# Kernel optimization log

Hardware: AMD Instinct MI355X
Metric: run time of the kernel (lower is better)

Reference implementation:

```python
import jax, jax.numpy as jnp
import numpy as np

ALPHA = 1.0
RANK = 4


def _conv2d_same(x, w):
    # x: [B,C,H,W], w: [O,C,kh,kw], stride 1, 'same' padding
    return jax.lax.conv_general_dilated(
        x, w, window_strides=(1, 1), padding='SAME',
        dimension_numbers=('NCHW', 'OIHW', 'NCHW'))


def setup_inputs() -> dict:
    key = jax.random.key(0)
    k1, k2, k3, k4, k5 = jax.random.split(key, 5)
    B, C, H, W = 32, 64, 64, 256
    O, E, r, k = 64, 4, RANK, 3
    x = jax.random.normal(k1, (B, C, H, W), dtype=jnp.float32)
    subject_id = jax.random.randint(k2, (B,), 0, E, dtype=jnp.int64)
    W_conv = jax.random.normal(k3, (O, C, k, k), dtype=jnp.float32) * (1.0 / np.sqrt(C * k * k))
    W_A = jax.random.normal(k4, (E, r, C, k, k), dtype=jnp.float32) * 0.02
    # torch init zeros W_B; use random here so the LoRA path is numerically exercised
    W_B = jax.random.normal(k5, (E, O, r), dtype=jnp.float32) * 0.02
    return {'x': x, 'subject_id': subject_id, 'W_conv': W_conv, 'W_A': W_A, 'W_B': W_B}


def reference(x, subject_id, W_conv, W_A, W_B):
    B, C, H, W = x.shape
    E, r = W_A.shape[0], W_A.shape[1]
    k = W_A.shape[-1]
    # Base conv
    out = _conv2d_same(x, W_conv)  # [B,O,H,W]
    # Run all adapter A-convs in one batched conv (E*r tiny output channels),
    # then per-sample select the adapter matching subject_id (same math as the
    # masked per-adapter dispatch in the original).
    a_all = _conv2d_same(x, W_A.reshape(E * r, C, k, k))  # [B,E*r,H,W]
    a_all = a_all.reshape(B, E, r, H, W)
    idx = subject_id[:, None, None, None, None]
    a_sel = jnp.take_along_axis(a_all, idx, axis=1)[:, 0]  # [B,r,H,W]
    wb_sel = W_B[subject_id]  # [B,O,r] (1x1 conv weight per sample)
    lora = (ALPHA / r) * jnp.einsum('bor,brhw->bohw', wb_sel, a_sel)
    return out + lora
```

## Files before the change

kernel.cpp:

```cpp
#include <hip/hip_runtime.h>
#include <hip/hip_bf16.h>

typedef __attribute__((ext_vector_type(8)))  short bf16x8;
typedef __attribute__((ext_vector_type(16))) float f32x16;

constexpr int Bn = 32, Cn = 64, Hn = 64, Wn = 256, On = 64, En = 4, Rn = 4;
constexpr float SCALE = 1.0f / Rn;

constexpr int ROW_B  = 258 * 128;

constexpr int WTILE  = 64;
constexpr int HSTRIP = 8;
constexpr int SLOT_B = 66 * 128;

constexpr size_t WFRAG_B = 294912;
constexpr size_t XP_B    = (size_t)Bn * Hn * ROW_B;
constexpr size_t ZROW_B  = ROW_B;

#define GLOAD_LDS16(SRC, DST) \
    __builtin_amdgcn_global_load_lds( \
        (const __attribute__((address_space(1))) void*)(SRC), \
        (__attribute__((address_space(3))) void*)(DST), 16, 0, 0)

__global__ __launch_bounds__(256) void merge_k(
    const float* __restrict__ Wc, const float* __restrict__ Wa,
    const float* __restrict__ Wb, __hip_bfloat16* __restrict__ Wfrag)
{
    int t = blockIdx.x * 256 + threadIdx.x;
    int j    = t & 7;
    int lane = (t >> 3) & 63;
    int g    = t >> 9;
    int s    = g % 36;
    int mh   = (g / 36) & 1;
    int e    = g / 72;
    int m = lane & 31, half = lane >> 5;
    int o = mh * 32 + m;
    int tap = s >> 2, cq = s & 3;
    int c = cq * 16 + half * 8 + j;
    float acc = Wc[(o * Cn + c) * 9 + tap];
#pragma unroll
    for (int r = 0; r < Rn; ++r)
        acc += SCALE * Wb[(e * On + o) * Rn + r] * Wa[((e * Rn + r) * Cn + c) * 9 + tap];
    Wfrag[t] = __float2bfloat16(acc);
}

__global__ __launch_bounds__(256) void pack2_k(
    const float* __restrict__ x, __hip_bfloat16* __restrict__ xp,
    __hip_bfloat16* __restrict__ zr)
{
    const int blk = blockIdx.x;
    if (blk < 4096) {
        int l  = ((blk & 1) << 8) | threadIdx.x;
        int bh = blk >> 1;
        int wLo = l & 3, cb = (l >> 2) & 7, wHi = l >> 5;
        int wq = wHi * 4 + wLo;
        int b = bh >> 6, h = bh & 63;
        const float* src = x + (((size_t)(b * Cn + cb * 8) * Hn + h) * Wn) + 4 * wq;
        float4 f[8];
#pragma unroll
        for (int i = 0; i < 8; ++i)
            f[i] = *reinterpret_cast<const float4*>(src + (size_t)i * Hn * Wn);
        char* row = (char*)xp + (size_t)bh * ROW_B;
#pragma unroll
        for (int j = 0; j < 4; ++j) {
            union { __hip_bfloat16 u[8]; bf16x8 v; } pk;
#pragma unroll
            for (int i = 0; i < 8; ++i) {
                float v = (j == 0) ? f[i].x : (j == 1) ? f[i].y : (j == 2) ? f[i].z : f[i].w;
                pk.u[i] = __float2bfloat16(v);
            }
            int s = 4 * wq + 1 + j;
            *reinterpret_cast<bf16x8*>(row + s * 128 + ((cb ^ (s & 7)) * 16)) = pk.v;
        }
    } else if (blk < 4096 + 128) {
        int z = (blk - 4096) * 256 + threadIdx.x;
        int cb = z & 7, t = (z >> 3) & 1, bh = z >> 4;
        char* row = (char*)xp + (size_t)bh * ROW_B;
        bf16x8 zz = {};
        *reinterpret_cast<bf16x8*>(row + (t ? 257 : 0) * 128 + cb * 16) = zz;
    } else {
        int t = (blk - 4096 - 128) * 256 + threadIdx.x;
        if (t < ROW_B / 16) {
            bf16x8 zz = {};
            reinterpret_cast<bf16x8*>(zr)[t] = zz;
        }
    }
}

__global__ __launch_bounds__(256, 2) void conv10_k(
    const __hip_bfloat16* __restrict__ xp, const __hip_bfloat16* __restrict__ zr,
    const int* __restrict__ sid, const __hip_bfloat16* __restrict__ Wfrag,
    float* __restrict__ out)
{
    __shared__ __align__(16) char xs[4 * SLOT_B];

    const int logical = ((blockIdx.x & 7) << 7) | (blockIdx.x >> 3);
    const int bx = logical & 3, by = (logical >> 2) & 7, b = logical >> 5;

    const int tid = threadIdx.x;
    const int w0  = bx * WTILE;
    const int h0  = by * HSTRIP;
    const int e   = sid[b];
    const size_t HW = (size_t)Hn * Wn;

    const int lane = tid & 63, wave = tid >> 6;
    const int mh = wave & 1, nh = wave >> 1;
    const int n = lane & 31, half = lane >> 5;

    bf16x8 wf[36];
    const bf16x8* wg = reinterpret_cast<const bf16x8*>(Wfrag) + (size_t)(e * 2 + mh) * 36 * 64;
#pragma unroll
    for (int s = 0; s < 36; ++s) wf[s] = wg[s * 64 + lane];

    const char* xpb = (const char*)xp + (size_t)b * Hn * ROW_B + (size_t)w0 * 128;
    const char* zrw = (const char*)zr + (size_t)w0 * 128;
    const int lofs = wave * 1024 + lane * 16;

    auto stage = [&](int rx) {
        const int gh = h0 + rx;
        const char* src = ((unsigned)gh < (unsigned)Hn) ? (xpb + (size_t)gh * ROW_B) : zrw;
        char* dst = xs + ((rx + 1) & 3) * SLOT_B + wave * 1024;
        GLOAD_LDS16(src + lofs,        dst);
        GLOAD_LDS16(src + 4096 + lofs, dst + 4096);
        GLOAD_LDS16(src + 4352 + lofs, dst + 4352);
    };

    stage(-1); stage(0); stage(1);
    asm volatile("s_waitcnt vmcnt(0) lgkmcnt(0)" ::: "memory");
    __builtin_amdgcn_s_barrier();

    for (int st = 0; st < HSTRIP; ++st) {
        stage(st + 2);
        asm volatile("" ::: "memory");

        f32x16 a0, a1;
#pragma unroll
        for (int i = 0; i < 16; ++i) { a0[i] = 0.0f; a1[i] = 0.0f; }

#pragma unroll
        for (int s2 = 0; s2 < 18; ++s2) {
            {
                const int s = 2 * s2;
                const int tap = s >> 2, cq = s & 3;
                const int dh = tap / 3, dw = tap % 3;
                int ww = nh * 32 + n + dw;
                const char* p = xs + ((st + dh) & 3) * SLOT_B
                              + ww * 128 + (((cq * 2 + half) ^ (ww & 7)) * 16);
                a0 = __builtin_amdgcn_mfma_f32_32x32x16_bf16(
                        wf[s], *reinterpret_cast<const bf16x8*>(p), a0, 0, 0, 0);
            }
            {
                const int s = 2 * s2 + 1;
                const int tap = s >> 2, cq = s & 3;
                const int dh = tap / 3, dw = tap % 3;
                int ww = nh * 32 + n + dw;
                const char* p = xs + ((st + dh) & 3) * SLOT_B
                              + ww * 128 + (((cq * 2 + half) ^ (ww & 7)) * 16);
                a1 = __builtin_amdgcn_mfma_f32_32x32x16_bf16(
                        wf[s], *reinterpret_cast<const bf16x8*>(p), a1, 0, 0, 0);
            }
        }

        {
            const int hrow = h0 + st;
            size_t base = ((size_t)(b * On + mh * 32 + 4 * half) * Hn + hrow) * Wn
                          + w0 + nh * 32 + n;
#pragma unroll
            for (int r = 0; r < 16; ++r) {
                int o_off = (r & 3) + 8 * (r >> 2);
                out[base + (size_t)o_off * HW] = a0[r] + a1[r];
            }
        }

        asm volatile("s_waitcnt vmcnt(16) lgkmcnt(0)" ::: "memory");
        __builtin_amdgcn_s_barrier();
    }
}

constexpr int FB_WTILE  = 32;
constexpr int FB_HSTRIP = 16;
constexpr int FB_SLOT_B = 34 * 128;

__device__ __forceinline__ int fb_swz(int ww, int cb) {
    return ww * 128 + ((cb ^ ((ww >> 2) & 7)) * 16);
}

__global__ __launch_bounds__(128, 2) void conv8_k(
    const float* __restrict__ x, const int* __restrict__ sid,
    const __hip_bfloat16* __restrict__ Wfrag, float* __restrict__ out)
{
    __shared__ __align__(16) char xs[4 * FB_SLOT_B];

    const int tid = threadIdx.x;
    const int w0  = blockIdx.x * FB_WTILE;
    const int h0  = blockIdx.y * FB_HSTRIP;
    const int b   = blockIdx.z;
    const int e   = sid[b];
    const size_t HW = (size_t)Hn * Wn;

    const int lane = tid & 63, mh = tid >> 6;
    const int n = lane & 31, half = lane >> 5;

    bf16x8 wf[36];
    const bf16x8* wg = reinterpret_cast<const bf16x8*>(Wfrag) + (size_t)(e * 2 + mh) * 36 * 64;
#pragma unroll
    for (int s = 0; s < 36; ++s) wf[s] = wg[s * 64 + lane];

    const int pb = tid >> 3, q = tid & 7;
    const float* xbase = x + ((size_t)b * Cn + pb * 4) * HW + w0 + 4 * q;

    const int hside = tid >> 6, hc = tid & 63;
    const int gwh   = hside ? (w0 + FB_WTILE) : (w0 - 1);
    const bool hv   = (unsigned)gwh < (unsigned)Wn;
    const float* hbase = x + ((size_t)b * Cn + hc) * HW + gwh;

    auto stage_load = [&](float4 (&f)[4], float& hx, int rx) {
        const int gh = h0 + rx;
        if ((unsigned)gh < (unsigned)Hn) {
            const float* src = xbase + (size_t)gh * Wn;
#pragma unroll
            for (int r = 0; r < 4; ++r)
                f[r] = *reinterpret_cast<const float4*>(src + r * HW);
            hx = hv ? hbase[(size_t)gh * Wn] : 0.0f;
        } else {
            float4 z4 = make_float4(0.0f, 0.0f, 0.0f, 0.0f);
#pragma unroll
            for (int r = 0; r < 4; ++r) f[r] = z4;
            hx = 0.0f;
        }
    };
    auto stage_store = [&](float4 (&f)[4], float& hx, int rx) {
        const int slot = (rx + 1) & 3;
        char* dbase = xs + slot * FB_SLOT_B;
        const int cb = pb >> 1, sub = (pb & 1) * 8;
#pragma unroll
        for (int j = 0; j < 4; ++j) {
            union { __hip_bfloat16 u[4]; short4 v; } pk;
#pragma unroll
            for (int r = 0; r < 4; ++r) {
                float v = (j == 0) ? f[r].x : (j == 1) ? f[r].y : (j == 2) ? f[r].z : f[r].w;
                pk.u[r] = __float2bfloat16(v);
            }
            int ww = 4 * q + 1 + j;
            *reinterpret_cast<short4*>(dbase + fb_swz(ww, cb) + sub) = pk.v;
        }
        {
            __hip_bfloat16 hb = __float2bfloat16(hx);
            int ww = hside ? (FB_WTILE + 1) : 0;
            *reinterpret_cast<__hip_bfloat16*>(dbase + fb_swz(ww, hc >> 3) + (hc & 7) * 2) = hb;
        }
    };

    auto barrier = [&]() {
        asm volatile("s_waitcnt lgkmcnt(0)" ::: "memory");
        __builtin_amdgcn_s_barrier();
    };

    float4 fA[4], fB[4];
    float  hxA, hxB;

    stage_load(fA, hxA, -1); stage_store(fA, hxA, -1);
    stage_load(fA, hxA, 0);  stage_store(fA, hxA, 0);
    stage_load(fA, hxA, 1);  stage_store(fA, hxA, 1);
    stage_load(fA, hxA, 2);
    barrier();

    for (int st = 0; st < FB_HSTRIP; ++st) {
        const bool do_issue = (st + 3 <= FB_HSTRIP);
        if (do_issue) {
            if (st & 1) stage_load(fA, hxA, st + 3);
            else        stage_load(fB, hxB, st + 3);
        }

        f32x16 a;
#pragma unroll
        for (int i = 0; i < 16; ++i) a[i] = 0.0f;

#pragma unroll
        for (int s = 0; s < 36; ++s) {
            const int tap = s >> 2, cq = s & 3;
            const int dh = tap / 3, dw = tap % 3;
            const int slotbase = ((st + dh) & 3) * FB_SLOT_B;
            int ww = n + dw;
            bf16x8 bf = *reinterpret_cast<const bf16x8*>(xs + slotbase + fb_swz(ww, cq * 2 + half));
            a = __builtin_amdgcn_mfma_f32_32x32x16_bf16(wf[s], bf, a, 0, 0, 0);
        }

        const bool do_store = (st + 2 <= FB_HSTRIP);
        if (do_store) {
            if (st & 1) stage_store(fB, hxB, st + 2);
            else        stage_store(fA, hxA, st + 2);
        }

        {
            const int hrow = h0 + st;
            size_t base = ((size_t)(b * On + mh * 32 + 4 * half) * Hn + hrow) * Wn + w0 + n;
#pragma unroll
            for (int r = 0; r < 16; ++r) {
                int o_off = (r & 3) + 8 * (r >> 2);
                out[base + (size_t)o_off * HW] = a[r];
            }
        }

        barrier();
    }
}

extern "C" void kernel_launch(void* const* d_in, const int* in_sizes, int n_in,
                              void* d_out, int out_size, void* d_ws, size_t ws_size,
                              hipStream_t stream)
{
    const float* x   = (const float*)d_in[0];
    const int*   sid = (const int*)d_in[1];
    const float* Wc  = (const float*)d_in[2];
    const float* Wa  = (const float*)d_in[3];
    const float* Wb  = (const float*)d_in[4];
    float*       out = (float*)d_out;

    __hip_bfloat16* Wfrag = (__hip_bfloat16*)d_ws;

    merge_k<<<En * 2 * 36 * 64 * 8 / 256, 256, 0, stream>>>(Wc, Wa, Wb, Wfrag);

    const size_t NEED = WFRAG_B + XP_B + ZROW_B;
    if (ws_size >= NEED) {
        __hip_bfloat16* xp = (__hip_bfloat16*)((char*)d_ws + WFRAG_B);
        __hip_bfloat16* zw = (__hip_bfloat16*)((char*)d_ws + WFRAG_B + XP_B);
        pack2_k<<<4096 + 128 + 9, 256, 0, stream>>>(x, xp, zw);
        conv10_k<<<dim3(1024, 1, 1), 256, 0, stream>>>(xp, zw, sid, Wfrag, out);
    } else {
        dim3 grid(Wn / FB_WTILE, Hn / FB_HSTRIP, Bn);
        conv8_k<<<grid, 128, 0, stream>>>(x, sid, Wfrag, out);
    }
}
```

Before: 277.4 us.

## Compute two output rows per iteration sharing LDS loads, double strip height

The conv kernel now processes two output rows per loop iteration. Each input-row fragment is read from LDS once and fed to the MFMAs of both rows, which roughly halves LDS reads per output. The H-strip grows to 16 rows with an 8-slot LDS ring, two rows are prefetched per iteration, and the grid shrinks to 512 blocks, which cuts halo row reloads. The costs are twice the LDS footprint, fewer blocks to fill the GPU, and a deeper vmcnt wait that must match the larger number of loads in flight.

Result: no change. 278.7 us (+0.5%).

```diff
diff --git a/kernel.cpp b/kernel.cpp
--- a/kernel.cpp
+++ b/kernel.cpp
@@ -10,7 +10,7 @@
 constexpr int ROW_B  = 258 * 128;
 
 constexpr int WTILE  = 64;
-constexpr int HSTRIP = 8;
+constexpr int HSTRIP = 16;
 constexpr int SLOT_B = 66 * 128;
 
 constexpr size_t WFRAG_B = 294912;
@@ -87,15 +87,16 @@
     }
 }
 
-__global__ __launch_bounds__(256, 2) void conv10_k(
+__global__ __launch_bounds__(256, 2) void conv11_k(
     const __hip_bfloat16* __restrict__ xp, const __hip_bfloat16* __restrict__ zr,
     const int* __restrict__ sid, const __hip_bfloat16* __restrict__ Wfrag,
     float* __restrict__ out)
 {
-    __shared__ __align__(16) char xs[4 * SLOT_B];
-
-    const int logical = ((blockIdx.x & 7) << 7) | (blockIdx.x >> 3);
-    const int bx = logical & 3, by = (logical >> 2) & 7, b = logical >> 5;
+    __shared__ __align__(16) char xs[8 * SLOT_B];
+
+    const int logical = ((blockIdx.x & 7) << 6) | (blockIdx.x >> 3);
+    const int tile = logical & 15;
+    const int bx = tile & 3, by = tile >> 2, b = logical >> 4;
 
     const int tid = threadIdx.x;
     const int w0  = bx * WTILE;
@@ -119,60 +120,59 @@
     auto stage = [&](int rx) {
         const int gh = h0 + rx;
         const char* src = ((unsigned)gh < (unsigned)Hn) ? (xpb + (size_t)gh * ROW_B) : zrw;
-        char* dst = xs + ((rx + 1) & 3) * SLOT_B + wave * 1024;
+        char* dst = xs + ((rx + 1) & 7) * SLOT_B + wave * 1024;
         GLOAD_LDS16(src + lofs,        dst);
         GLOAD_LDS16(src + 4096 + lofs, dst + 4096);
         GLOAD_LDS16(src + 4352 + lofs, dst + 4352);
     };
 
-    stage(-1); stage(0); stage(1);
+    stage(-1); stage(0); stage(1); stage(2);
     asm volatile("s_waitcnt vmcnt(0) lgkmcnt(0)" ::: "memory");
     __builtin_amdgcn_s_barrier();
 
-    for (int st = 0; st < HSTRIP; ++st) {
-        stage(st + 2);
+    for (int st = 0; st < HSTRIP; st += 2) {
+        if (st + 4 <= HSTRIP) { stage(st + 3); stage(st + 4); }
         asm volatile("" ::: "memory");
 
-        f32x16 a0, a1;
-#pragma unroll
-        for (int i = 0; i < 16; ++i) { a0[i] = 0.0f; a1[i] = 0.0f; }
-
-#pragma unroll
-        for (int s2 = 0; s2 < 18; ++s2) {
-            {
-                const int s = 2 * s2;
-                const int tap = s >> 2, cq = s & 3;
-                const int dh = tap / 3, dw = tap % 3;
-                int ww = nh * 32 + n + dw;
-                const char* p = xs + ((st + dh) & 3) * SLOT_B
-                              + ww * 128 + (((cq * 2 + half) ^ (ww & 7)) * 16);
-                a0 = __builtin_amdgcn_mfma_f32_32x32x16_bf16(
-                        wf[s], *reinterpret_cast<const bf16x8*>(p), a0, 0, 0, 0);
-            }
-            {
-                const int s = 2 * s2 + 1;
-                const int tap = s >> 2, cq = s & 3;
-                const int dh = tap / 3, dw = tap % 3;
-                int ww = nh * 32 + n + dw;
-                const char* p = xs + ((st + dh) & 3) * SLOT_B
-                              + ww * 128 + (((cq * 2 + half) ^ (ww & 7)) * 16);
-                a1 = __builtin_amdgcn_mfma_f32_32x32x16_bf16(
-                        wf[s], *reinterpret_cast<const bf16x8*>(p), a1, 0, 0, 0);
+        f32x16 aA, aB;
+#pragma unroll
+        for (int i = 0; i < 16; ++i) { aA[i] = 0.0f; aB[i] = 0.0f; }
+
+#pragma unroll
+        for (int k = 0; k < 4; ++k) {
+            const int slotbase = ((st + k) & 7) * SLOT_B;
+#pragma unroll
+            for (int dw = 0; dw < 3; ++dw) {
+                const int ww = nh * 32 + n + dw;
+                const char* pbase = xs + slotbase + ww * 128;
+#pragma unroll
+                for (int cq = 0; cq < 4; ++cq) {
+                    bf16x8 bf = *reinterpret_cast<const bf16x8*>(
+                        pbase + (((cq * 2 + half) ^ (ww & 7)) * 16));
+                    if (k <= 2) {
+                        const int s = (k * 3 + dw) * 4 + cq;
+                        aA = __builtin_amdgcn_mfma_f32_32x32x16_bf16(wf[s], bf, aA, 0, 0, 0);
+                    }
+                    if (k >= 1) {
+                        const int s = ((k - 1) * 3 + dw) * 4 + cq;
+                        aB = __builtin_amdgcn_mfma_f32_32x32x16_bf16(wf[s], bf, aB, 0, 0, 0);
+                    }
+                }
             }
         }
 
         {
-            const int hrow = h0 + st;
-            size_t base = ((size_t)(b * On + mh * 32 + 4 * half) * Hn + hrow) * Wn
+            size_t base = ((size_t)(b * On + mh * 32 + 4 * half) * Hn + (h0 + st)) * Wn
                           + w0 + nh * 32 + n;
 #pragma unroll
             for (int r = 0; r < 16; ++r) {
                 int o_off = (r & 3) + 8 * (r >> 2);
-                out[base + (size_t)o_off * HW] = a0[r] + a1[r];
-            }
-        }
-
-        asm volatile("s_waitcnt vmcnt(16) lgkmcnt(0)" ::: "memory");
+                out[base + (size_t)o_off * HW]      = aA[r];
+                out[base + (size_t)o_off * HW + Wn] = aB[r];
+            }
+        }
+
+        asm volatile("s_waitcnt vmcnt(32) lgkmcnt(0)" ::: "memory");
         __builtin_amdgcn_s_barrier();
     }
 }
@@ -326,7 +326,7 @@
         __hip_bfloat16* xp = (__hip_bfloat16*)((char*)d_ws + WFRAG_B);
         __hip_bfloat16* zw = (__hip_bfloat16*)((char*)d_ws + WFRAG_B + XP_B);
         pack2_k<<<4096 + 128 + 9, 256, 0, stream>>>(x, xp, zw);
-        conv10_k<<<dim3(1024, 1, 1), 256, 0, stream>>>(xp, zw, sid, Wfrag, out);
+        conv11_k<<<dim3(512, 1, 1), 256, 0, stream>>>(xp, zw, sid, Wfrag, out);
     } else {
         dim3 grid(Wn / FB_WTILE, Hn / FB_HSTRIP, Bn);
         conv8_k<<<grid, 128, 0, stream>>>(x, sid, Wfrag, out);
```

## Fuse weight merge into pack kernel and deepen LDS row prefetch to six slots

Applied to the files above, without the earlier changes.

Folds the weight-merge kernel into the input-pack prologue as extra blocks, which removes one kernel launch on the fast path. The conv kernel's LDS ring goes from four to six row slots and prefetches three rows ahead instead of two, to hide more global-to-LDS latency. The cost is more LDS per block, which may limit occupancy. The hidden wait-count logic must also match the new prefetch depth.

Measured after the change: 290.4 us. 1.05x slower.

```diff
diff --git a/kernel.cpp b/kernel.cpp
--- a/kernel.cpp
+++ b/kernel.cpp
@@ -12,6 +12,7 @@
 constexpr int WTILE  = 64;
 constexpr int HSTRIP = 8;
 constexpr int SLOT_B = 66 * 128;
+constexpr int NSLOT  = 6;
 
 constexpr size_t WFRAG_B = 294912;
 constexpr size_t XP_B    = (size_t)Bn * Hn * ROW_B;
@@ -22,11 +23,10 @@
         (const __attribute__((address_space(1))) void*)(SRC), \
         (__attribute__((address_space(3))) void*)(DST), 16, 0, 0)
 
-__global__ __launch_bounds__(256) void merge_k(
-    const float* __restrict__ Wc, const float* __restrict__ Wa,
+__device__ __forceinline__ void merge_body(
+    int t, const float* __restrict__ Wc, const float* __restrict__ Wa,
     const float* __restrict__ Wb, __hip_bfloat16* __restrict__ Wfrag)
 {
-    int t = blockIdx.x * 256 + threadIdx.x;
     int j    = t & 7;
     int lane = (t >> 3) & 63;
     int g    = t >> 9;
@@ -44,9 +44,18 @@
     Wfrag[t] = __float2bfloat16(acc);
 }
 
-__global__ __launch_bounds__(256) void pack2_k(
+__global__ __launch_bounds__(256) void merge_k(
+    const float* __restrict__ Wc, const float* __restrict__ Wa,
+    const float* __restrict__ Wb, __hip_bfloat16* __restrict__ Wfrag)
+{
+    merge_body(blockIdx.x * 256 + threadIdx.x, Wc, Wa, Wb, Wfrag);
+}
+
+__global__ __launch_bounds__(256) void prologue_k(
     const float* __restrict__ x, __hip_bfloat16* __restrict__ xp,
-    __hip_bfloat16* __restrict__ zr)
+    __hip_bfloat16* __restrict__ zr,
+    const float* __restrict__ Wc, const float* __restrict__ Wa,
+    const float* __restrict__ Wb, __hip_bfloat16* __restrict__ Wfrag)
 {
     const int blk = blockIdx.x;
     if (blk < 4096) {
@@ -78,21 +87,23 @@
         char* row = (char*)xp + (size_t)bh * ROW_B;
         bf16x8 zz = {};
         *reinterpret_cast<bf16x8*>(row + (t ? 257 : 0) * 128 + cb * 16) = zz;
-    } else {
+    } else if (blk < 4096 + 128 + 9) {
         int t = (blk - 4096 - 128) * 256 + threadIdx.x;
         if (t < ROW_B / 16) {
             bf16x8 zz = {};
             reinterpret_cast<bf16x8*>(zr)[t] = zz;
         }
+    } else {
+        merge_body((blk - 4233) * 256 + threadIdx.x, Wc, Wa, Wb, Wfrag);
     }
 }
 
-__global__ __launch_bounds__(256, 2) void conv10_k(
+__global__ __launch_bounds__(256, 2) void conv12_k(
     const __hip_bfloat16* __restrict__ xp, const __hip_bfloat16* __restrict__ zr,
     const int* __restrict__ sid, const __hip_bfloat16* __restrict__ Wfrag,
     float* __restrict__ out)
 {
-    __shared__ __align__(16) char xs[4 * SLOT_B];
+    __shared__ __align__(16) char xs[NSLOT * SLOT_B];
 
     const int logical = ((blockIdx.x & 7) << 7) | (blockIdx.x >> 3);
     const int bx = logical & 3, by = (logical >> 2) & 7, b = logical >> 5;
@@ -116,21 +127,23 @@
     const char* zrw = (const char*)zr + (size_t)w0 * 128;
     const int lofs = wave * 1024 + lane * 16;
 
+    auto m6 = [](int v) { return v >= NSLOT ? v - NSLOT : v; };
+
     auto stage = [&](int rx) {
         const int gh = h0 + rx;
         const char* src = ((unsigned)gh < (unsigned)Hn) ? (xpb + (size_t)gh * ROW_B) : zrw;
-        char* dst = xs + ((rx + 1) & 3) * SLOT_B + wave * 1024;
+        char* dst = xs + m6(rx + 1) * SLOT_B + wave * 1024;
         GLOAD_LDS16(src + lofs,        dst);
         GLOAD_LDS16(src + 4096 + lofs, dst + 4096);
         GLOAD_LDS16(src + 4352 + lofs, dst + 4352);
     };
 
-    stage(-1); stage(0); stage(1);
+    stage(-1); stage(0); stage(1); stage(2);
     asm volatile("s_waitcnt vmcnt(0) lgkmcnt(0)" ::: "memory");
     __builtin_amdgcn_s_barrier();
 
     for (int st = 0; st < HSTRIP; ++st) {
-        stage(st + 2);
+        if (st + 3 <= HSTRIP) stage(st + 3);
         asm volatile("" ::: "memory");
 
         f32x16 a0, a1;
@@ -144,7 +157,7 @@
                 const int tap = s >> 2, cq = s & 3;
                 const int dh = tap / 3, dw = tap % 3;
                 int ww = nh * 32 + n + dw;
-                const char* p = xs + ((st + dh) & 3) * SLOT_B
+                const char* p = xs + m6(st + dh) * SLOT_B
                               + ww * 128 + (((cq * 2 + half) ^ (ww & 7)) * 16);
                 a0 = __builtin_amdgcn_mfma_f32_32x32x16_bf16(
                         wf[s], *reinterpret_cast<const bf16x8*>(p), a0, 0, 0, 0);
@@ -154,7 +167,7 @@
                 const int tap = s >> 2, cq = s & 3;
                 const int dh = tap / 3, dw = tap % 3;
                 int ww = nh * 32 + n + dw;
-                const char* p = xs + ((st + dh) & 3) * SLOT_B
+                const char* p = xs + m6(st + dh) * SLOT_B
                               + ww * 128 + (((cq * 2 + half) ^ (ww & 7)) * 16);
                 a1 = __builtin_amdgcn_mfma_f32_32x32x16_bf16(
                         wf[s], *reinterpret_cast<const bf16x8*>(p), a1, 0, 0, 0);
@@ -319,15 +332,14 @@
 
     __hip_bfloat16* Wfrag = (__hip_bfloat16*)d_ws;
 
-    merge_k<<<En * 2 * 36 * 64 * 8 / 256, 256, 0, stream>>>(Wc, Wa, Wb, Wfrag);
-
     const size_t NEED = WFRAG_B + XP_B + ZROW_B;
     if (ws_size >= NEED) {
         __hip_bfloat16* xp = (__hip_bfloat16*)((char*)d_ws + WFRAG_B);
         __hip_bfloat16* zw = (__hip_bfloat16*)((char*)d_ws + WFRAG_B + XP_B);
-        pack2_k<<<4096 + 128 + 9, 256, 0, stream>>>(x, xp, zw);
-        conv10_k<<<dim3(1024, 1, 1), 256, 0, stream>>>(xp, zw, sid, Wfrag, out);
+        prologue_k<<<4096 + 128 + 9 + 576, 256, 0, stream>>>(x, xp, zw, Wc, Wa, Wb, Wfrag);
+        conv12_k<<<dim3(1024, 1, 1), 256, 0, stream>>>(xp, zw, sid, Wfrag, out);
     } else {
+        merge_k<<<En * 2 * 36 * 64 * 8 / 256, 256, 0, stream>>>(Wc, Wa, Wb, Wfrag);
         dim3 grid(Wn / FB_WTILE, Hn / FB_HSTRIP, Bn);
         conv8_k<<<grid, 128, 0, stream>>>(x, sid, Wfrag, out);
     }
```

## Split conv reduction over channels across two wave groups with LDS partial-sum exchange

Applied to the files above, without the earlier changes.

Doubles the conv block to 512 threads. The input-channel reduction is split between two wave groups, each keeping half the weight fragments in registers and running 18 MFMAs per row instead of 36. The second group writes its partial accumulators to a new LDS buffer, and the first group adds them before storing the output. This lowers register pressure and raises waves per CU to hide latency, but adds an extra barrier per row, LDS traffic, and idle waves during the store phase.

After: 279.5 us. No clear change (+0.8%).

```diff
diff --git a/kernel.cpp b/kernel.cpp
--- a/kernel.cpp
+++ b/kernel.cpp
@@ -12,6 +12,7 @@
 constexpr int WTILE  = 64;
 constexpr int HSTRIP = 8;
 constexpr int SLOT_B = 66 * 128;
+constexpr int PB_STR = 80;
 
 constexpr size_t WFRAG_B = 294912;
 constexpr size_t XP_B    = (size_t)Bn * Hn * ROW_B;
@@ -87,12 +88,13 @@
     }
 }
 
-__global__ __launch_bounds__(256, 2) void conv10_k(
+__global__ __launch_bounds__(512, 4) void conv13_k(
     const __hip_bfloat16* __restrict__ xp, const __hip_bfloat16* __restrict__ zr,
     const int* __restrict__ sid, const __hip_bfloat16* __restrict__ Wfrag,
     float* __restrict__ out)
 {
     __shared__ __align__(16) char xs[4 * SLOT_B];
+    __shared__ __align__(16) char pbuf[4 * 64 * PB_STR];
 
     const int logical = ((blockIdx.x & 7) << 7) | (blockIdx.x >> 3);
     const int bx = logical & 3, by = (logical >> 2) & 7, b = logical >> 5;
@@ -104,13 +106,16 @@
     const size_t HW = (size_t)Hn * Wn;
 
     const int lane = tid & 63, wave = tid >> 6;
-    const int mh = wave & 1, nh = wave >> 1;
+    const int mh = wave & 1, nh = (wave >> 1) & 1, kh = wave >> 2;
     const int n = lane & 31, half = lane >> 5;
 
-    bf16x8 wf[36];
+    bf16x8 wf[18];
     const bf16x8* wg = reinterpret_cast<const bf16x8*>(Wfrag) + (size_t)(e * 2 + mh) * 36 * 64;
 #pragma unroll
-    for (int s = 0; s < 36; ++s) wf[s] = wg[s * 64 + lane];
+    for (int tap = 0; tap < 9; ++tap)
+#pragma unroll
+        for (int cqq = 0; cqq < 2; ++cqq)
+            wf[tap * 2 + cqq] = wg[(tap * 4 + kh * 2 + cqq) * 64 + lane];
 
     const char* xpb = (const char*)xp + (size_t)b * Hn * ROW_B + (size_t)w0 * 128;
     const char* zrw = (const char*)zr + (size_t)w0 * 128;
@@ -125,54 +130,66 @@
         GLOAD_LDS16(src + 4352 + lofs, dst + 4352);
     };
 
-    stage(-1); stage(0); stage(1);
-    asm volatile("s_waitcnt vmcnt(0) lgkmcnt(0)" ::: "memory");
+    char* pb = pbuf + ((wave & 3) * 64 + lane) * PB_STR;
+
+    if (kh == 0) {
+        stage(-1); stage(0); stage(1);
+        asm volatile("s_waitcnt vmcnt(0) lgkmcnt(0)" ::: "memory");
+    }
     __builtin_amdgcn_s_barrier();
 
     for (int st = 0; st < HSTRIP; ++st) {
-        stage(st + 2);
+        if (kh == 0) stage(st + 2);
         asm volatile("" ::: "memory");
 
-        f32x16 a0, a1;
-#pragma unroll
-        for (int i = 0; i < 16; ++i) { a0[i] = 0.0f; a1[i] = 0.0f; }
-
-#pragma unroll
-        for (int s2 = 0; s2 < 18; ++s2) {
-            {
-                const int s = 2 * s2;
-                const int tap = s >> 2, cq = s & 3;
-                const int dh = tap / 3, dw = tap % 3;
-                int ww = nh * 32 + n + dw;
-                const char* p = xs + ((st + dh) & 3) * SLOT_B
-                              + ww * 128 + (((cq * 2 + half) ^ (ww & 7)) * 16);
-                a0 = __builtin_amdgcn_mfma_f32_32x32x16_bf16(
-                        wf[s], *reinterpret_cast<const bf16x8*>(p), a0, 0, 0, 0);
-            }
-            {
-                const int s = 2 * s2 + 1;
-                const int tap = s >> 2, cq = s & 3;
-                const int dh = tap / 3, dw = tap % 3;
-                int ww = nh * 32 + n + dw;
-                const char* p = xs + ((st + dh) & 3) * SLOT_B
-                              + ww * 128 + (((cq * 2 + half) ^ (ww & 7)) * 16);
-                a1 = __builtin_amdgcn_mfma_f32_32x32x16_bf16(
-                        wf[s], *reinterpret_cast<const bf16x8*>(p), a1, 0, 0, 0);
-            }
-        }
-
-        {
+        f32x16 a;
+#pragma unroll
+        for (int i = 0; i < 16; ++i) a[i] = 0.0f;
+
+#pragma unroll
+        for (int tap = 0; tap < 9; ++tap) {
+            const int dh = tap / 3, dw = tap % 3;
+            const int slotbase = ((st + dh) & 3) * SLOT_B;
+            const int ww = nh * 32 + n + dw;
+            const char* pbase = xs + slotbase + ww * 128;
+#pragma unroll
+            for (int cqq = 0; cqq < 2; ++cqq) {
+                const int cg = (kh * 2 + cqq) * 2 + half;
+                bf16x8 bf = *reinterpret_cast<const bf16x8*>(
+                    pbase + ((cg ^ (ww & 7)) * 16));
+                a = __builtin_amdgcn_mfma_f32_32x32x16_bf16(wf[tap * 2 + cqq], bf, a, 0, 0, 0);
+            }
+        }
+
+        if (kh == 1) {
+#pragma unroll
+            for (int k = 0; k < 4; ++k) {
+                float4 v = make_float4(a[4 * k + 0], a[4 * k + 1], a[4 * k + 2], a[4 * k + 3]);
+                *reinterpret_cast<float4*>(pb + k * 16) = v;
+            }
+        }
+        asm volatile("s_waitcnt lgkmcnt(0)" ::: "memory");
+        __builtin_amdgcn_s_barrier();
+
+        if (kh == 0) {
             const int hrow = h0 + st;
             size_t base = ((size_t)(b * On + mh * 32 + 4 * half) * Hn + hrow) * Wn
                           + w0 + nh * 32 + n;
 #pragma unroll
-            for (int r = 0; r < 16; ++r) {
-                int o_off = (r & 3) + 8 * (r >> 2);
-                out[base + (size_t)o_off * HW] = a0[r] + a1[r];
-            }
-        }
-
-        asm volatile("s_waitcnt vmcnt(16) lgkmcnt(0)" ::: "memory");
+            for (int k = 0; k < 4; ++k) {
+                float4 p = *reinterpret_cast<const float4*>(pb + k * 16);
+#pragma unroll
+                for (int q = 0; q < 4; ++q) {
+                    int r = 4 * k + q;
+                    int o_off = (r & 3) + 8 * (r >> 2);
+                    float pv = (q == 0) ? p.x : (q == 1) ? p.y : (q == 2) ? p.z : p.w;
+                    out[base + (size_t)o_off * HW] = a[r] + pv;
+                }
+            }
+            asm volatile("s_waitcnt vmcnt(16) lgkmcnt(0)" ::: "memory");
+        } else {
+            asm volatile("s_waitcnt lgkmcnt(0)" ::: "memory");
+        }
         __builtin_amdgcn_s_barrier();
     }
 }
@@ -326,7 +343,7 @@
         __hip_bfloat16* xp = (__hip_bfloat16*)((char*)d_ws + WFRAG_B);
         __hip_bfloat16* zw = (__hip_bfloat16*)((char*)d_ws + WFRAG_B + XP_B);
         pack2_k<<<4096 + 128 + 9, 256, 0, stream>>>(x, xp, zw);
-        conv10_k<<<dim3(1024, 1, 1), 256, 0, stream>>>(xp, zw, sid, Wfrag, out);
+        conv13_k<<<dim3(1024, 1, 1), 512, 0, stream>>>(xp, zw, sid, Wfrag, out);
     } else {
         dim3 grid(Wn / FB_WTILE, Hn / FB_HSTRIP, Bn);
         conv8_k<<<grid, 128, 0, stream>>>(x, sid, Wfrag, out);
```
